# Kernel tuning notes

Hardware: AMD Instinct MI355X
Metric: run time of the kernel (lower is better)

## Reference

```python
import jax, jax.numpy as jnp
import numpy as np

NUM_CODES = 1024
CODE_DIM = 64
EMA_DECAY = 0.99
COMMIT_W = 0.25
EPS = 1e-5
B = 262144


def setup_inputs() -> dict:
    key = jax.random.key(0)
    k1, k2, k3, k4 = jax.random.split(key, 4)
    z = jax.random.normal(k1, (B, CODE_DIM), dtype=jnp.float32)
    weight = jax.random.normal(k2, (NUM_CODES, CODE_DIM), dtype=jnp.float32)
    ema_cluster_size = jax.random.uniform(k3, (NUM_CODES,), dtype=jnp.float32)
    ema_embed_sum = jax.random.normal(k4, (NUM_CODES, CODE_DIM), dtype=jnp.float32)
    return {"z": z, "weight": weight, "ema_cluster_size": ema_cluster_size,
            "ema_embed_sum": ema_embed_sum}


def reference(z, weight, ema_cluster_size, ema_embed_sum):
    # Squared Euclidean distances (argmin equivalent to cdist argmin)
    # d2[b,k] = ||z_b||^2 - 2 z_b . w_k + ||w_k||^2
    z2 = jnp.sum(z * z, axis=-1, keepdims=True)          # (B, 1)
    w2 = jnp.sum(weight * weight, axis=-1)               # (K,)
    d2 = z2 - 2.0 * (z @ weight.T) + w2[None, :]         # (B, K)
    indices = jnp.argmin(d2, axis=-1)                    # (B,)
    z_q = weight[indices]                                # gather with OLD weights

    # EMA codebook update (training, ema_update=True)
    ones = jnp.ones((z.shape[0],), dtype=z.dtype)
    cluster_size = jax.ops.segment_sum(ones, indices, num_segments=NUM_CODES)
    embed_sum = jax.ops.segment_sum(z, indices, num_segments=NUM_CODES)
    new_cs = EMA_DECAY * ema_cluster_size + (1.0 - EMA_DECAY) * cluster_size
    new_es = EMA_DECAY * ema_embed_sum + (1.0 - EMA_DECAY) * embed_sum
    n = jnp.sum(new_cs)
    smoothed = (new_cs + EPS) / (n + NUM_CODES * EPS) * n
    new_weight = new_es / smoothed[:, None]

    # commitment loss (z detached in torch; pure value here)
    vq_loss = COMMIT_W * jnp.mean((z - z_q) ** 2)

    # straight-through estimator
    z_q_st = z + jax.lax.stop_gradient(z_q - z)
    return z_q_st, indices, vq_loss, new_cs, new_es, new_weight
```

## Files before the change

### kernel.cpp

```cpp
#include <hip/hip_runtime.h>

typedef __attribute__((ext_vector_type(8))) short bf16x8;
typedef __attribute__((ext_vector_type(4))) float f32x4;

#define B_ROWS 262144
#define K_CODES 1024
#define DIM 64
#define DELTA 0.015f
#define ESPLIT 8

#define OUT_ZQ 0
#define OUT_IDX 16777216
#define OUT_LOSS 17039360
#define OUT_NEWCS 17039361
#define OUT_NEWES 17040385
#define OUT_NEWW 17105921

#define WS_LOSS   0
#define WS_QCOUNT 1
#define WS_W2     16
#define WS_SMOOTH 1056
#define WS_WHI    2080
#define WS_WLO    34848
#define WS_CPART  67616
#define WS_EPART  75808
#define WS_MINI   600096
#define WS_QUEUE  862240

static __device__ __forceinline__ unsigned short f2bf(float x) {
    unsigned u = __float_as_uint(x);
    unsigned r = (u + 0x7fffu + ((u >> 16) & 1u)) >> 16;
    return (unsigned short)r;
}
static __device__ __forceinline__ float bf2f(unsigned short u) {
    return __uint_as_float(((unsigned)u) << 16);
}

__global__ __launch_bounds__(256) void vq_w2_kernel(const float* __restrict__ w,
                                                    float* __restrict__ w2) {
    int k = blockIdx.x * 256 + threadIdx.x;
    if (k < K_CODES) {
        const float4* w4 = (const float4*)(w + (size_t)k * DIM);
        float s = 0.f;
#pragma unroll
        for (int j = 0; j < 16; ++j) {
            float4 v = w4[j];
            s += v.x * v.x + v.y * v.y + v.z * v.z + v.w * v.w;
        }
        w2[k] = s;
    }
}

__global__ __launch_bounds__(256) void vq_wcvt_kernel(const float* __restrict__ w,
                                                      float* __restrict__ ws) {
    int i = blockIdx.x * 256 + threadIdx.x;
    ushort4* whi = (ushort4*)(ws + WS_WHI);
    ushort4* wlo = (ushort4*)(ws + WS_WLO);
    float4 v = ((const float4*)w)[i];
    ushort4 h, l;
    h.x = f2bf(v.x); l.x = f2bf(v.x - bf2f(h.x));
    h.y = f2bf(v.y); l.y = f2bf(v.y - bf2f(h.y));
    h.z = f2bf(v.z); l.z = f2bf(v.z - bf2f(h.z));
    h.w = f2bf(v.w); l.w = f2bf(v.w - bf2f(h.w));
    whi[i] = h;
    wlo[i] = l;
}

static __device__ __forceinline__ void cvt_frag(const float* zrow, bf16x8& hi, bf16x8& lo) {
    float4 f0 = *(const float4*)zrow;
    float4 f1 = *(const float4*)(zrow + 4);
    float tf[8] = {f0.x, f0.y, f0.z, f0.w, f1.x, f1.y, f1.z, f1.w};
#pragma unroll
    for (int j = 0; j < 8; ++j) {
        unsigned short h = f2bf(tf[j]);
        hi[j] = (short)h;
        lo[j] = (short)f2bf(tf[j] - bf2f(h));
    }
}

__global__ __launch_bounds__(256) void vq_screen_kernel(
    const float* __restrict__ z, float* __restrict__ ws) {
    __shared__ __align__(16) unsigned short lds_h[128 * 72];
    __shared__ __align__(16) unsigned short lds_l[128 * 72];
    __shared__ float lds_w2[K_CODES];

    int tid = threadIdx.x;
    int l = tid & 63, q = l >> 4, m = l & 15;
    int wave = tid >> 6;

    *(float4*)&lds_w2[tid * 4] = ((const float4*)(ws + WS_W2))[tid];

    int row0 = blockIdx.x * 128 + wave * 32 + m;
    bf16x8 ahi[2][2], alo[2][2];
#pragma unroll
    for (int g = 0; g < 2; ++g) {
        const float* zr = z + (size_t)(row0 + g * 16) * DIM + q * 8;
        cvt_frag(zr, ahi[g][0], alo[g][0]);
        cvt_frag(zr + 32, ahi[g][1], alo[g][1]);
    }

    float mv[8], m2[8];
    int mi[8];
#pragma unroll
    for (int v = 0; v < 8; ++v) { mv[v] = 3.4e38f; m2[v] = 3.4e38f; mi[v] = 0; }

    const uint4* gh = (const uint4*)(ws + WS_WHI);
    const uint4* gl = (const uint4*)(ws + WS_WLO);

    for (int cch = 0; cch < 8; ++cch) {
        if (cch) __syncthreads();
#pragma unroll
        for (int j = 0; j < 4; ++j) {
            int chunk = tid + j * 256;
            int r = chunk >> 3, c8 = chunk & 7;
            *(uint4*)&lds_h[r * 72 + c8 * 8] = gh[cch * 1024 + chunk];
            *(uint4*)&lds_l[r * 72 + c8 * 8] = gl[cch * 1024 + chunk];
        }
        __syncthreads();

#pragma unroll 2
        for (int tg = 0; tg < 8; ++tg) {
            int cl = tg * 16 + m;
            bf16x8 bhi0 = *(const bf16x8*)&lds_h[cl * 72 + q * 8];
            bf16x8 bhi1 = *(const bf16x8*)&lds_h[cl * 72 + 32 + q * 8];
            bf16x8 blo0 = *(const bf16x8*)&lds_l[cl * 72 + q * 8];
            bf16x8 blo1 = *(const bf16x8*)&lds_l[cl * 72 + 32 + q * 8];
            float w2v = lds_w2[cch * 128 + tg * 16 + m];
            int cg = cch * 128 + tg * 16 + m;
#pragma unroll
            for (int g = 0; g < 2; ++g) {
                f32x4 acc = {0.f, 0.f, 0.f, 0.f};
                acc = __builtin_amdgcn_mfma_f32_16x16x32_bf16(alo[g][0], bhi0, acc, 0, 0, 0);
                acc = __builtin_amdgcn_mfma_f32_16x16x32_bf16(ahi[g][0], blo0, acc, 0, 0, 0);
                acc = __builtin_amdgcn_mfma_f32_16x16x32_bf16(alo[g][1], bhi1, acc, 0, 0, 0);
                acc = __builtin_amdgcn_mfma_f32_16x16x32_bf16(ahi[g][1], blo1, acc, 0, 0, 0);
                acc = __builtin_amdgcn_mfma_f32_16x16x32_bf16(ahi[g][0], bhi0, acc, 0, 0, 0);
                acc = __builtin_amdgcn_mfma_f32_16x16x32_bf16(ahi[g][1], bhi1, acc, 0, 0, 0);
#pragma unroll
                for (int r = 0; r < 4; ++r) {
                    int v = g * 4 + r;
                    float d = fmaf(acc[r], -2.0f, w2v);
                    bool lt = d < mv[v];
                    m2[v] = lt ? mv[v] : fminf(d, m2[v]);
                    mv[v] = lt ? d : mv[v];
                    mi[v] = lt ? cg : mi[v];
                }
            }
        }
    }

#pragma unroll
    for (int o = 1; o < 16; o <<= 1) {
#pragma unroll
        for (int v = 0; v < 8; ++v) {
            float ov = __shfl_xor(mv[v], o, 64);
            float ov2 = __shfl_xor(m2[v], o, 64);
            int oi = __shfl_xor(mi[v], o, 64);
            float nm2 = fminf(fminf(m2[v], ov2), fmaxf(mv[v], ov));
            bool take = (ov < mv[v]) || (ov == mv[v] && oi < mi[v]);
            mv[v] = take ? ov : mv[v];
            mi[v] = take ? oi : mi[v];
            m2[v] = nm2;
        }
    }
    if (m == 0) {
#pragma unroll
        for (int v = 0; v < 8; ++v) {
            int g = v >> 2, r = v & 3;
            int row = blockIdx.x * 128 + wave * 32 + g * 16 + q * 4 + r;
            bool amb = (m2[v] - mv[v] <= DELTA);
            ((int*)ws)[WS_MINI + row] = mi[v] | (amb ? 0x80000000 : 0);
        }
    }
}

__global__ __launch_bounds__(256) void vq_gather_kernel(
    const float* __restrict__ z, const float* __restrict__ w,
    float* __restrict__ ws, float* __restrict__ out) {
    __shared__ float lred[4];
    int tid = threadIdx.x;
    int row = blockIdx.x * 256 + tid;
    int enc = ((const int*)ws)[WS_MINI + row];
    float lsum = 0.f;
    if (enc >= 0) {
        int mi = enc;
        out[OUT_IDX + row] = (float)mi;
        const float4* zp = (const float4*)(z + (size_t)row * DIM);
        const float4* wq4 = (const float4*)(w + (size_t)mi * DIM);
        float4* outp = (float4*)(out + OUT_ZQ + (size_t)row * DIM);
#pragma unroll
        for (int j = 0; j < 16; ++j) {
            float4 x = zp[j];
            float4 qv = wq4[j];
            float4 st;
            st.x = x.x + (qv.x - x.x);
            st.y = x.y + (qv.y - x.y);
            st.z = x.z + (qv.z - x.z);
            st.w = x.w + (qv.w - x.w);
            outp[j] = st;
            float e0 = x.x - qv.x, e1 = x.y - qv.y, e2 = x.z - qv.z, e3 = x.w - qv.w;
            lsum += e0 * e0;
            lsum += e1 * e1;
            lsum += e2 * e2;
            lsum += e3 * e3;
        }
    } else {
        int pos = atomicAdd((int*)ws + WS_QCOUNT, 1);
        ((int*)ws)[WS_QUEUE + pos] = row;
    }
#pragma unroll
    for (int o = 32; o; o >>= 1) lsum += __shfl_down(lsum, o, 64);
    if ((tid & 63) == 0) lred[tid >> 6] = lsum;
    __syncthreads();
    if (tid == 0) atomicAdd(ws + WS_LOSS, lred[0] + lred[1] + lred[2] + lred[3]);
}

__global__ __launch_bounds__(256) void vq_fixup_kernel(
    const float* __restrict__ z, const float* __restrict__ w,
    float* __restrict__ ws, float* __restrict__ out) {
    const float* __restrict__ w2 = ws + WS_W2;
    int count = ((const int*)ws)[WS_QCOUNT];
    int lane = threadIdx.x & 63;
    int wv = (blockIdx.x * 256 + threadIdx.x) >> 6;
    int nw = (gridDim.x * 256) >> 6;
    for (int qi = wv; qi < count; qi += nw) {
        int row = ((const int*)ws)[WS_QUEUE + qi];
        const float* zr = z + (size_t)row * DIM;
        float zloc[DIM];
#pragma unroll
        for (int d = 0; d < DIM; ++d) zloc[d] = zr[d];
        float z2 = 0.f;
#pragma unroll
        for (int d = 0; d < DIM; ++d) z2 = fmaf(zloc[d], zloc[d], z2);
        float best = 3.4e38f;
        int bi = 0;
        for (int i = 0; i < 16; ++i) {
            int c = i * 64 + lane;
            const float* wr = w + (size_t)c * DIM;
            float a = 0.f;
#pragma unroll
            for (int d = 0; d < DIM; ++d) a = fmaf(zloc[d], wr[d], a);
            float dd = (z2 - 2.f * a) + w2[c];
            if (dd < best) { best = dd; bi = c; }
        }
#pragma unroll
        for (int o = 1; o < 64; o <<= 1) {
            float ov = __shfl_xor(best, o, 64);
            int oi = __shfl_xor(bi, o, 64);
            if (ov < best || (ov == best && oi < bi)) { best = ov; bi = oi; }
        }
        float x = zr[lane];
        float qv = w[(size_t)bi * DIM + lane];
        out[OUT_ZQ + (size_t)row * DIM + lane] = x + (qv - x);
        float e = x - qv;
        float s = e * e;
#pragma unroll
        for (int o = 32; o; o >>= 1) s += __shfl_down(s, o, 64);
        if (lane == 0) {
            out[OUT_IDX + row] = (float)bi;
            atomicAdd(ws + WS_LOSS, s);
        }
    }
}

__global__ __launch_bounds__(256) void vq_embed_kernel(
    const float* __restrict__ z, const float* __restrict__ idx_f,
    float* __restrict__ ws) {
    int code = blockIdx.x & (K_CODES - 1);
    int split = blockIdx.x >> 10;
    float code_f = (float)code;
    int tid = threadIdx.x;
    int wave = tid >> 6, lane = tid & 63;

    float acc = 0.f;
    float cnt = 0.f;

    const float4* idx4 = (const float4*)idx_f;
    int base0 = split * (B_ROWS / ESPLIT);
    for (int i = 0; i < B_ROWS / (ESPLIT * 1024); ++i) {
        int base = base0 + i * 1024 + wave * 256;
        float4 f = idx4[(base >> 2) + lane];
        unsigned long long m0 = __ballot(f.x == code_f);
        unsigned long long m1 = __ballot(f.y == code_f);
        unsigned long long m2 = __ballot(f.z == code_f);
        unsigned long long m3 = __ballot(f.w == code_f);
        cnt += (f.x == code_f) + (f.y == code_f) + (f.z == code_f) + (f.w == code_f);
        while (m0) { int b = __ffsll(m0) - 1; m0 &= m0 - 1;
            acc += z[(size_t)(base + 4 * b + 0) * DIM + lane]; }
        while (m1) { int b = __ffsll(m1) - 1; m1 &= m1 - 1;
            acc += z[(size_t)(base + 4 * b + 1) * DIM + lane]; }
        while (m2) { int b = __ffsll(m2) - 1; m2 &= m2 - 1;
            acc += z[(size_t)(base + 4 * b + 2) * DIM + lane]; }
        while (m3) { int b = __ffsll(m3) - 1; m3 &= m3 - 1;
            acc += z[(size_t)(base + 4 * b + 3) * DIM + lane]; }
    }

    __shared__ float red[4][DIM];
    __shared__ float cred[4];
    red[wave][lane] = acc;
#pragma unroll
    for (int o = 32; o; o >>= 1) cnt += __shfl_down(cnt, o, 64);
    if (lane == 0) cred[wave] = cnt;
    __syncthreads();
    if (wave == 0) {
        float s = red[0][lane] + red[1][lane] + red[2][lane] + red[3][lane];
        ws[WS_EPART + split * (K_CODES * DIM) + (size_t)code * DIM + lane] = s;
        if (lane == 0)
            ws[WS_CPART + split * K_CODES + code] = cred[0] + cred[1] + cred[2] + cred[3];
    }
}

__global__ __launch_bounds__(1024) void vq_finalize1_kernel(
    const float* __restrict__ ema_cs, float* __restrict__ ws,
    float* __restrict__ out) {
    int k = threadIdx.x;
    float c = 0.f;
#pragma unroll
    for (int j = 0; j < ESPLIT; ++j) c += ws[WS_CPART + j * K_CODES + k];
    float nc = 0.99f * ema_cs[k] + 0.01f * c;
    out[OUT_NEWCS + k] = nc;

    float s = nc;
#pragma unroll
    for (int o = 32; o; o >>= 1) s += __shfl_down(s, o, 64);
    __shared__ float red[16];
    __shared__ float n_sh;
    if ((k & 63) == 0) red[k >> 6] = s;
    __syncthreads();
    if (k == 0) {
        float n = 0.f;
#pragma unroll
        for (int i = 0; i < 16; ++i) n += red[i];
        n_sh = n;
        out[OUT_LOSS] = 0.25f * (ws[WS_LOSS] / 16777216.0f);
    }
    __syncthreads();
    float n = n_sh;
    ws[WS_SMOOTH + k] = (nc + 1e-5f) / (n + 0.01024f) * n;
}

__global__ __launch_bounds__(256) void vq_finalize2_kernel(
    const float* __restrict__ ema_es, const float* __restrict__ ws,
    float* __restrict__ out) {
    int i = blockIdx.x * 256 + threadIdx.x;
    int k = i >> 6;
    float e = 0.f;
#pragma unroll
    for (int j = 0; j < ESPLIT; ++j) e += ws[WS_EPART + j * 65536 + i];
    float es = 0.99f * ema_es[i] + 0.01f * e;
    out[OUT_NEWES + i] = es;
    out[OUT_NEWW + i] = es / ws[WS_SMOOTH + k];
}

extern "C" void kernel_launch(void* const* d_in, const int* in_sizes, int n_in,
                              void* d_out, int out_size, void* d_ws, size_t ws_size,
                              hipStream_t stream) {
    const float* z = (const float*)d_in[0];
    const float* weight = (const float*)d_in[1];
    const float* ema_cs = (const float*)d_in[2];
    const float* ema_es = (const float*)d_in[3];
    float* out = (float*)d_out;
    float* ws = (float*)d_ws;

    hipMemsetAsync(ws, 0, 64, stream);
    vq_w2_kernel<<<4, 256, 0, stream>>>(weight, ws + WS_W2);
    vq_wcvt_kernel<<<64, 256, 0, stream>>>(weight, ws);
    vq_screen_kernel<<<B_ROWS / 128, 256, 0, stream>>>(z, ws);
    vq_gather_kernel<<<B_ROWS / 256, 256, 0, stream>>>(z, weight, ws, out);
    vq_fixup_kernel<<<128, 256, 0, stream>>>(z, weight, ws, out);
    vq_embed_kernel<<<ESPLIT * K_CODES, 256, 0, stream>>>(z, out + OUT_IDX, ws);
    vq_finalize1_kernel<<<1, 1024, 0, stream>>>(ema_cs, ws, out);
    vq_finalize2_kernel<<<256, 256, 0, stream>>>(ema_es, ws, out);
}
```

Baseline: 448.6 us.

## Rework screen MFMA tiling, prefetch codebook, and bin-based embed accumulation

The screening kernel now uses 32x32x16 bf16 MFMAs with a pre-swizzled LDS layout, and it register-prefetches the next codebook chunk while the current one is computed. The w2 and bf16 split-conversion kernels are merged into one prep kernel. The per-code embed kernel, which scanned all indices for each of 1024 codes across 8 splits, is replaced by 256 blocks that each cover a 128-code range over a row slice and accumulate into LDS with atomics. The finalize kernels are adapted to the new partial layout, and the fixup grid is doubled. The aim is to cut the redundant index scanning in the embed stage and raise MFMA efficiency, at the cost of LDS atomic contention and a larger partial-sum workspace.

```diff
diff --git a/kernel.cpp b/kernel.cpp
--- a/kernel.cpp
+++ b/kernel.cpp
@@ -1,13 +1,12 @@
 #include <hip/hip_runtime.h>
 
 typedef __attribute__((ext_vector_type(8))) short bf16x8;
-typedef __attribute__((ext_vector_type(4))) float f32x4;
+typedef __attribute__((ext_vector_type(16))) float f32x16;
 
 #define B_ROWS 262144
 #define K_CODES 1024
 #define DIM 64
 #define DELTA 0.015f
-#define ESPLIT 8
 
 #define OUT_ZQ 0
 #define OUT_IDX 16777216
@@ -19,157 +18,150 @@
 #define WS_LOSS   0
 #define WS_QCOUNT 1
 #define WS_W2     16
-#define WS_SMOOTH 1056
-#define WS_WHI    2080
-#define WS_WLO    34848
-#define WS_CPART  67616
-#define WS_EPART  75808
-#define WS_MINI   600096
-#define WS_QUEUE  862240
+#define WS_SMOOTH 1040
+#define WS_WHI    2064
+#define WS_WLO    34832
+#define WS_CPART  67600
+#define WS_EPART  100368
+#define WS_MINI   2197520
+#define WS_QUEUE  2459664
 
 static __device__ __forceinline__ unsigned short f2bf(float x) {
     unsigned u = __float_as_uint(x);
-    unsigned r = (u + 0x7fffu + ((u >> 16) & 1u)) >> 16;
-    return (unsigned short)r;
+    return (unsigned short)((u + 0x7fffu + ((u >> 16) & 1u)) >> 16);
 }
 static __device__ __forceinline__ float bf2f(unsigned short u) {
     return __uint_as_float(((unsigned)u) << 16);
 }
 
-__global__ __launch_bounds__(256) void vq_w2_kernel(const float* __restrict__ w,
-                                                    float* __restrict__ w2) {
-    int k = blockIdx.x * 256 + threadIdx.x;
-    if (k < K_CODES) {
-        const float4* w4 = (const float4*)(w + (size_t)k * DIM);
-        float s = 0.f;
-#pragma unroll
-        for (int j = 0; j < 16; ++j) {
-            float4 v = w4[j];
-            s += v.x * v.x + v.y * v.y + v.z * v.z + v.w * v.w;
-        }
-        w2[k] = s;
-    }
-}
-
-__global__ __launch_bounds__(256) void vq_wcvt_kernel(const float* __restrict__ w,
-                                                      float* __restrict__ ws) {
-    int i = blockIdx.x * 256 + threadIdx.x;
-    ushort4* whi = (ushort4*)(ws + WS_WHI);
-    ushort4* wlo = (ushort4*)(ws + WS_WLO);
-    float4 v = ((const float4*)w)[i];
+__global__ __launch_bounds__(256) void vq_prep(const float* __restrict__ w,
+                                               float* __restrict__ ws) {
+    int i4 = blockIdx.x * 256 + threadIdx.x;
+    float4 v = ((const float4*)w)[i4];
     ushort4 h, l;
     h.x = f2bf(v.x); l.x = f2bf(v.x - bf2f(h.x));
     h.y = f2bf(v.y); l.y = f2bf(v.y - bf2f(h.y));
     h.z = f2bf(v.z); l.z = f2bf(v.z - bf2f(h.z));
     h.w = f2bf(v.w); l.w = f2bf(v.w - bf2f(h.w));
-    whi[i] = h;
-    wlo[i] = l;
-}
-
-static __device__ __forceinline__ void cvt_frag(const float* zrow, bf16x8& hi, bf16x8& lo) {
-    float4 f0 = *(const float4*)zrow;
-    float4 f1 = *(const float4*)(zrow + 4);
-    float tf[8] = {f0.x, f0.y, f0.z, f0.w, f1.x, f1.y, f1.z, f1.w};
-#pragma unroll
-    for (int j = 0; j < 8; ++j) {
-        unsigned short h = f2bf(tf[j]);
-        hi[j] = (short)h;
-        lo[j] = (short)f2bf(tf[j] - bf2f(h));
-    }
-}
-
-__global__ __launch_bounds__(256) void vq_screen_kernel(
+    ((ushort4*)(ws + WS_WHI))[i4] = h;
+    ((ushort4*)(ws + WS_WLO))[i4] = l;
+    float s = v.x * v.x + v.y * v.y + v.z * v.z + v.w * v.w;
+    s += __shfl_xor(s, 1, 64);
+    s += __shfl_xor(s, 2, 64);
+    s += __shfl_xor(s, 4, 64);
+    s += __shfl_xor(s, 8, 64);
+    if ((threadIdx.x & 15) == 0) ws[WS_W2 + (i4 >> 4)] = s;
+}
+
+__global__ __launch_bounds__(256, 3) void vq_screen_kernel(
     const float* __restrict__ z, float* __restrict__ ws) {
-    __shared__ __align__(16) unsigned short lds_h[128 * 72];
-    __shared__ __align__(16) unsigned short lds_l[128 * 72];
+    __shared__ __align__(16) unsigned short lds_h[8192];
+    __shared__ __align__(16) unsigned short lds_l[8192];
     __shared__ float lds_w2[K_CODES];
 
     int tid = threadIdx.x;
-    int l = tid & 63, q = l >> 4, m = l & 15;
-    int wave = tid >> 6;
+    int l = tid & 63, wave = tid >> 6;
+    int col = l & 31, hh = l >> 5;
 
     *(float4*)&lds_w2[tid * 4] = ((const float4*)(ws + WS_W2))[tid];
 
-    int row0 = blockIdx.x * 128 + wave * 32 + m;
-    bf16x8 ahi[2][2], alo[2][2];
-#pragma unroll
-    for (int g = 0; g < 2; ++g) {
-        const float* zr = z + (size_t)(row0 + g * 16) * DIM + q * 8;
-        cvt_frag(zr, ahi[g][0], alo[g][0]);
-        cvt_frag(zr + 32, ahi[g][1], alo[g][1]);
-    }
-
-    float mv[8], m2[8];
-    int mi[8];
-#pragma unroll
-    for (int v = 0; v < 8; ++v) { mv[v] = 3.4e38f; m2[v] = 3.4e38f; mi[v] = 0; }
+    int rowbase = blockIdx.x * 128 + wave * 32;
+    const float* zr = z + (size_t)(rowbase + col) * DIM + hh * 8;
+    bf16x8 ahi[4], alo[4];
+#pragma unroll
+    for (int s = 0; s < 4; ++s) {
+        float4 f0 = *(const float4*)(zr + s * 16);
+        float4 f1 = *(const float4*)(zr + s * 16 + 4);
+        float tf[8] = {f0.x, f0.y, f0.z, f0.w, f1.x, f1.y, f1.z, f1.w};
+#pragma unroll
+        for (int j = 0; j < 8; ++j) {
+            unsigned short hb = f2bf(tf[j]);
+            ahi[s][j] = (short)hb;
+            alo[s][j] = (short)f2bf(tf[j] - bf2f(hb));
+        }
+    }
+
+    float mv[16], m2[16];
+    int mi[16];
+#pragma unroll
+    for (int r = 0; r < 16; ++r) { mv[r] = 3.4e38f; m2[r] = 3.4e38f; mi[r] = 0; }
 
     const uint4* gh = (const uint4*)(ws + WS_WHI);
     const uint4* gl = (const uint4*)(ws + WS_WLO);
 
+    uint4 ph[4], pl[4];
+#pragma unroll
+    for (int j = 0; j < 4; ++j) {
+        int G = j * 256 + tid;
+        int gidx = ((G >> 8) * 32 + (G & 31)) * 8 + ((G >> 6) & 3) * 2 + ((G >> 5) & 1);
+        ph[j] = gh[gidx];
+        pl[j] = gl[gidx];
+    }
+
     for (int cch = 0; cch < 8; ++cch) {
-        if (cch) __syncthreads();
+        __syncthreads();
 #pragma unroll
         for (int j = 0; j < 4; ++j) {
-            int chunk = tid + j * 256;
-            int r = chunk >> 3, c8 = chunk & 7;
-            *(uint4*)&lds_h[r * 72 + c8 * 8] = gh[cch * 1024 + chunk];
-            *(uint4*)&lds_l[r * 72 + c8 * 8] = gl[cch * 1024 + chunk];
+            *(uint4*)&lds_h[(unsigned)(j * 256 + tid) * 8] = ph[j];
+            *(uint4*)&lds_l[(unsigned)(j * 256 + tid) * 8] = pl[j];
         }
         __syncthreads();
-
-#pragma unroll 2
-        for (int tg = 0; tg < 8; ++tg) {
-            int cl = tg * 16 + m;
-            bf16x8 bhi0 = *(const bf16x8*)&lds_h[cl * 72 + q * 8];
-            bf16x8 bhi1 = *(const bf16x8*)&lds_h[cl * 72 + 32 + q * 8];
-            bf16x8 blo0 = *(const bf16x8*)&lds_l[cl * 72 + q * 8];
-            bf16x8 blo1 = *(const bf16x8*)&lds_l[cl * 72 + 32 + q * 8];
-            float w2v = lds_w2[cch * 128 + tg * 16 + m];
-            int cg = cch * 128 + tg * 16 + m;
-#pragma unroll
-            for (int g = 0; g < 2; ++g) {
-                f32x4 acc = {0.f, 0.f, 0.f, 0.f};
-                acc = __builtin_amdgcn_mfma_f32_16x16x32_bf16(alo[g][0], bhi0, acc, 0, 0, 0);
-                acc = __builtin_amdgcn_mfma_f32_16x16x32_bf16(ahi[g][0], blo0, acc, 0, 0, 0);
-                acc = __builtin_amdgcn_mfma_f32_16x16x32_bf16(alo[g][1], bhi1, acc, 0, 0, 0);
-                acc = __builtin_amdgcn_mfma_f32_16x16x32_bf16(ahi[g][1], blo1, acc, 0, 0, 0);
-                acc = __builtin_amdgcn_mfma_f32_16x16x32_bf16(ahi[g][0], bhi0, acc, 0, 0, 0);
-                acc = __builtin_amdgcn_mfma_f32_16x16x32_bf16(ahi[g][1], bhi1, acc, 0, 0, 0);
-#pragma unroll
-                for (int r = 0; r < 4; ++r) {
-                    int v = g * 4 + r;
-                    float d = fmaf(acc[r], -2.0f, w2v);
-                    bool lt = d < mv[v];
-                    m2[v] = lt ? mv[v] : fminf(d, m2[v]);
-                    mv[v] = lt ? d : mv[v];
-                    mi[v] = lt ? cg : mi[v];
-                }
+        if (cch < 7) {
+#pragma unroll
+            for (int j = 0; j < 4; ++j) {
+                int G = j * 256 + tid;
+                int gidx = ((cch + 1) * 128 + (G >> 8) * 32 + (G & 31)) * 8 +
+                           ((G >> 6) & 3) * 2 + ((G >> 5) & 1);
+                ph[j] = gh[gidx];
+                pl[j] = gl[gidx];
             }
         }
-    }
-
-#pragma unroll
-    for (int o = 1; o < 16; o <<= 1) {
-#pragma unroll
-        for (int v = 0; v < 8; ++v) {
-            float ov = __shfl_xor(mv[v], o, 64);
-            float ov2 = __shfl_xor(m2[v], o, 64);
-            int oi = __shfl_xor(mi[v], o, 64);
-            float nm2 = fminf(fminf(m2[v], ov2), fmaxf(mv[v], ov));
-            bool take = (ov < mv[v]) || (ov == mv[v] && oi < mi[v]);
-            mv[v] = take ? ov : mv[v];
-            mi[v] = take ? oi : mi[v];
-            m2[v] = nm2;
-        }
-    }
-    if (m == 0) {
-#pragma unroll
-        for (int v = 0; v < 8; ++v) {
-            int g = v >> 2, r = v & 3;
-            int row = blockIdx.x * 128 + wave * 32 + g * 16 + q * 4 + r;
-            bool amb = (m2[v] - mv[v] <= DELTA);
-            ((int*)ws)[WS_MINI + row] = mi[v] | (amb ? 0x80000000 : 0);
+
+#pragma unroll
+        for (int tl = 0; tl < 4; ++tl) {
+            f32x16 acc = {0.f, 0.f, 0.f, 0.f, 0.f, 0.f, 0.f, 0.f,
+                          0.f, 0.f, 0.f, 0.f, 0.f, 0.f, 0.f, 0.f};
+#pragma unroll
+            for (int s = 0; s < 4; ++s) {
+                bf16x8 bh = *(const bf16x8*)&lds_h[(unsigned)(tl * 256 + s * 64 + l) * 8];
+                bf16x8 bl = *(const bf16x8*)&lds_l[(unsigned)(tl * 256 + s * 64 + l) * 8];
+                acc = __builtin_amdgcn_mfma_f32_32x32x16_bf16(alo[s], bh, acc, 0, 0, 0);
+                acc = __builtin_amdgcn_mfma_f32_32x32x16_bf16(ahi[s], bl, acc, 0, 0, 0);
+                acc = __builtin_amdgcn_mfma_f32_32x32x16_bf16(ahi[s], bh, acc, 0, 0, 0);
+            }
+            int cg = cch * 128 + tl * 32 + col;
+            float w2v = lds_w2[cg];
+#pragma unroll
+            for (int r = 0; r < 16; ++r) {
+                float d = fmaf(acc[r], -2.0f, w2v);
+                bool lt = d < mv[r];
+                m2[r] = lt ? mv[r] : fminf(m2[r], d);
+                mv[r] = lt ? d : mv[r];
+                mi[r] = lt ? cg : mi[r];
+            }
+        }
+    }
+
+#pragma unroll
+    for (int o = 1; o < 32; o <<= 1) {
+#pragma unroll
+        for (int r = 0; r < 16; ++r) {
+            float ov = __shfl_xor(mv[r], o, 64);
+            float ov2 = __shfl_xor(m2[r], o, 64);
+            int oi = __shfl_xor(mi[r], o, 64);
+            float nm2 = fminf(fminf(m2[r], ov2), fmaxf(mv[r], ov));
+            bool take = (ov < mv[r]) || (ov == mv[r] && oi < mi[r]);
+            mv[r] = take ? ov : mv[r];
+            mi[r] = take ? oi : mi[r];
+            m2[r] = nm2;
+        }
+    }
+    if (col == 0) {
+#pragma unroll
+        for (int r = 0; r < 16; ++r) {
+            int row = rowbase + (r & 3) + 8 * (r >> 2) + 4 * hh;
+            bool amb = (m2[r] - mv[r] <= DELTA);
+            ((int*)ws)[WS_MINI + row] = mi[r] | (amb ? 0x80000000 : 0);
         }
     }
 }
@@ -266,57 +258,54 @@
 __global__ __launch_bounds__(256) void vq_embed_kernel(
     const float* __restrict__ z, const float* __restrict__ idx_f,
     float* __restrict__ ws) {
-    int code = blockIdx.x & (K_CODES - 1);
-    int split = blockIdx.x >> 10;
-    float code_f = (float)code;
+    __shared__ float eacc[128 * DIM];
+    __shared__ float ecnt[128];
+    int b = blockIdx.x;
+    int cs = b & 7, rs = b >> 3;
+    float lo = (float)(cs * 128), hi = (float)(cs * 128 + 128);
     int tid = threadIdx.x;
     int wave = tid >> 6, lane = tid & 63;
 
-    float acc = 0.f;
-    float cnt = 0.f;
+#pragma unroll
+    for (int j = 0; j < 32; ++j) eacc[j * 256 + tid] = 0.f;
+    if (tid < 128) ecnt[tid] = 0.f;
+    __syncthreads();
 
     const float4* idx4 = (const float4*)idx_f;
-    int base0 = split * (B_ROWS / ESPLIT);
-    for (int i = 0; i < B_ROWS / (ESPLIT * 1024); ++i) {
-        int base = base0 + i * 1024 + wave * 256;
+    for (int it = 0; it < 8; ++it) {
+        int base = rs * 8192 + wave * 2048 + it * 256;
         float4 f = idx4[(base >> 2) + lane];
-        unsigned long long m0 = __ballot(f.x == code_f);
-        unsigned long long m1 = __ballot(f.y == code_f);
-        unsigned long long m2 = __ballot(f.z == code_f);
-        unsigned long long m3 = __ballot(f.w == code_f);
-        cnt += (f.x == code_f) + (f.y == code_f) + (f.z == code_f) + (f.w == code_f);
-        while (m0) { int b = __ffsll(m0) - 1; m0 &= m0 - 1;
-            acc += z[(size_t)(base + 4 * b + 0) * DIM + lane]; }
-        while (m1) { int b = __ffsll(m1) - 1; m1 &= m1 - 1;
-            acc += z[(size_t)(base + 4 * b + 1) * DIM + lane]; }
-        while (m2) { int b = __ffsll(m2) - 1; m2 &= m2 - 1;
-            acc += z[(size_t)(base + 4 * b + 2) * DIM + lane]; }
-        while (m3) { int b = __ffsll(m3) - 1; m3 &= m3 - 1;
-            acc += z[(size_t)(base + 4 * b + 3) * DIM + lane]; }
-    }
-
-    __shared__ float red[4][DIM];
-    __shared__ float cred[4];
-    red[wave][lane] = acc;
-#pragma unroll
-    for (int o = 32; o; o >>= 1) cnt += __shfl_down(cnt, o, 64);
-    if (lane == 0) cred[wave] = cnt;
-    __syncthreads();
-    if (wave == 0) {
-        float s = red[0][lane] + red[1][lane] + red[2][lane] + red[3][lane];
-        ws[WS_EPART + split * (K_CODES * DIM) + (size_t)code * DIM + lane] = s;
-        if (lane == 0)
-            ws[WS_CPART + split * K_CODES + code] = cred[0] + cred[1] + cred[2] + cred[3];
-    }
+#pragma unroll
+        for (int c = 0; c < 4; ++c) {
+            float fv = (c == 0) ? f.x : (c == 1) ? f.y : (c == 2) ? f.z : f.w;
+            unsigned long long m = __ballot(fv >= lo && fv < hi);
+            while (m) {
+                int bb = __ffsll(m) - 1;
+                m &= m - 1;
+                int row = base + 4 * bb + c;
+                float cf = __shfl(fv, bb, 64);
+                int local = (int)cf - cs * 128;
+                float val = z[(size_t)row * DIM + lane];
+                atomicAdd(&eacc[local * DIM + lane], val);
+                if (lane == 0) atomicAdd(&ecnt[local], 1.f);
+            }
+        }
+    }
+    __syncthreads();
+#pragma unroll
+    for (int j = 0; j < 32; ++j)
+        ws[WS_EPART + (size_t)b * 8192 + j * 256 + tid] = eacc[j * 256 + tid];
+    if (tid < 128) ws[WS_CPART + b * 128 + tid] = ecnt[tid];
 }
 
 __global__ __launch_bounds__(1024) void vq_finalize1_kernel(
     const float* __restrict__ ema_cs, float* __restrict__ ws,
     float* __restrict__ out) {
     int k = threadIdx.x;
+    int cs = k >> 7, local = k & 127;
     float c = 0.f;
 #pragma unroll
-    for (int j = 0; j < ESPLIT; ++j) c += ws[WS_CPART + j * K_CODES + k];
+    for (int rs = 0; rs < 32; ++rs) c += ws[WS_CPART + (rs * 8 + cs) * 128 + local];
     float nc = 0.99f * ema_cs[k] + 0.01f * c;
     out[OUT_NEWCS + k] = nc;
 
@@ -343,13 +332,15 @@
     const float* __restrict__ ema_es, const float* __restrict__ ws,
     float* __restrict__ out) {
     int i = blockIdx.x * 256 + threadIdx.x;
-    int k = i >> 6;
+    int code = i >> 6, dim = i & 63;
+    int cs = code >> 7, local = code & 127;
     float e = 0.f;
 #pragma unroll
-    for (int j = 0; j < ESPLIT; ++j) e += ws[WS_EPART + j * 65536 + i];
+    for (int rs = 0; rs < 32; ++rs)
+        e += ws[WS_EPART + (size_t)(rs * 8 + cs) * 8192 + local * DIM + dim];
     float es = 0.99f * ema_es[i] + 0.01f * e;
     out[OUT_NEWES + i] = es;
-    out[OUT_NEWW + i] = es / ws[WS_SMOOTH + k];
+    out[OUT_NEWW + i] = es / ws[WS_SMOOTH + code];
 }
 
 extern "C" void kernel_launch(void* const* d_in, const int* in_sizes, int n_in,
@@ -363,12 +354,11 @@
     float* ws = (float*)d_ws;
 
     hipMemsetAsync(ws, 0, 64, stream);
-    vq_w2_kernel<<<4, 256, 0, stream>>>(weight, ws + WS_W2);
-    vq_wcvt_kernel<<<64, 256, 0, stream>>>(weight, ws);
+    vq_prep<<<64, 256, 0, stream>>>(weight, ws);
     vq_screen_kernel<<<B_ROWS / 128, 256, 0, stream>>>(z, ws);
     vq_gather_kernel<<<B_ROWS / 256, 256, 0, stream>>>(z, weight, ws, out);
-    vq_fixup_kernel<<<128, 256, 0, stream>>>(z, weight, ws, out);
-    vq_embed_kernel<<<ESPLIT * K_CODES, 256, 0, stream>>>(z, out + OUT_IDX, ws);
+    vq_fixup_kernel<<<256, 256, 0, stream>>>(z, weight, ws, out);
+    vq_embed_kernel<<<256, 256, 0, stream>>>(z, out + OUT_IDX, ws);
     vq_finalize1_kernel<<<1, 1024, 0, stream>>>(ema_cs, ws, out);
     vq_finalize2_kernel<<<256, 256, 0, stream>>>(ema_es, ws, out);
 }
```

Measured after the change: 1.100 ms. +145.2%, slower.
